# Performance work log

Hardware: AMD Instinct MI355X
Metric: run time of the kernel (lower is better)

## Reference

```python
import jax, jax.numpy as jnp
import numpy as np

K_HOPS = 2
IMPROVED = False  # self-loop fill weight = 1.0


def setup_inputs() -> dict:
    key = jax.random.key(0)
    k1, k2, k3 = jax.random.split(key, 3)
    n_nodes, n_edges, d_feat, units = 100000, 1600000, 64, 64
    x = jax.random.normal(k1, (n_nodes, d_feat), dtype=jnp.float32)
    edge_index = jax.random.randint(k2, (2, n_edges), 0, n_nodes, dtype=jnp.int32)
    edge_weight = jnp.ones((n_edges,), dtype=jnp.float32)
    kernel = jax.random.normal(k3, (d_feat, units), dtype=jnp.float32) * (1.0 / np.sqrt(d_feat))
    bias = jnp.zeros((units,), dtype=jnp.float32)
    return {"x": x, "edge_index": edge_index, "edge_weight": edge_weight,
            "kernel": kernel, "bias": bias}


def reference(x, edge_index, edge_weight, kernel, bias):
    n = x.shape[0]
    # renorm trick: add self-loops (fill=1, or 2 if improved) BEFORE normalization
    fill = jnp.float32(2.0 if IMPROVED else 1.0)
    loop_idx = jnp.arange(n, dtype=edge_index.dtype)
    row = jnp.concatenate([edge_index[0], loop_idx])
    col = jnp.concatenate([edge_index[1], loop_idx])
    w = jnp.concatenate([edge_weight, jnp.full((n,), fill, dtype=edge_weight.dtype)])
    # symmetric GCN normalization: D^{-1/2} A D^{-1/2}
    deg = jax.ops.segment_sum(w, row, num_segments=n)
    dinv = jnp.where(deg > 0, jax.lax.rsqrt(deg), 0.0)
    norm_w = dinv[row] * w * dinv[col]  # [n_edges + n]
    # K-hop propagation: gather source feats, scale, scatter-add to targets
    h = x
    for _ in range(K_HOPS):
        msgs = h[col] * norm_w[:, None]           # [E+n, d] gather + scale
        h = jax.ops.segment_sum(msgs, row, num_segments=n)  # scatter-add
    # final dense projection
    return h @ kernel + bias
```

## Files before the change

### kernel.cpp

```cpp
#include <hip/hip_runtime.h>

#define D 64

static __host__ __device__ inline int alignup(int x) { return (x + 63) & ~63; }

__device__ inline float blo(unsigned int u) { return __uint_as_float(u << 16); }
__device__ inline float bhi(unsigned int u) { return __uint_as_float(u & 0xffff0000u); }
__device__ inline unsigned short f2b(float f) {
    unsigned int u = __float_as_uint(f);
    return (unsigned short)((u + 0x7FFFu + ((u >> 16) & 1u)) >> 16);
}
__device__ inline unsigned int packb(float lo, float hi) {
    return (unsigned int)f2b(lo) | ((unsigned int)f2b(hi) << 16);
}

typedef short bf16x8 __attribute__((ext_vector_type(8)));
typedef float f32x4 __attribute__((ext_vector_type(4)));

__global__ void prep(const float* __restrict__ x, unsigned short* __restrict__ xb,
                     const float* __restrict__ W, unsigned short* __restrict__ wbt,
                     const int* __restrict__ row, int* __restrict__ bhist,
                     long nElem, int nbC, int E, int chunk, int NB) {
    int blk = (int)blockIdx.x;
    if (blk < nbC) {
        long t = (long)blk * blockDim.x + threadIdx.x;
        long i = t * 4;
        if (i + 3 < nElem) {
            float4 v = *(const float4*)(x + i);
            ushort4 o;
            o.x = f2b(v.x); o.y = f2b(v.y); o.z = f2b(v.z); o.w = f2b(v.w);
            *(ushort4*)(xb + i) = o;
        } else {
            for (long k = i; k < nElem; ++k) xb[k] = f2b(x[k]);
        }
        return;
    }
    if (blk < nbC + 16) {
        int idx = (blk - nbC) * 256 + threadIdx.x;
        int c = idx >> 6, k = idx & 63;
        wbt[c * 64 + k] = f2b(W[k * 64 + c]);
        return;
    }
    __shared__ int h[512];
    int b = blk - nbC - 16;
    for (int k = threadIdx.x; k < NB; k += blockDim.x) h[k] = 0;
    __syncthreads();
    int s = b * chunk, e = min(s + chunk, E);
    for (int p = s + (int)threadIdx.x; p < e; p += blockDim.x)
        atomicAdd(&h[row[p] >> 8], 1);
    __syncthreads();
    for (int k = threadIdx.x; k < NB; k += blockDim.x)
        bhist[k * 256 + b] = h[k];
}

__global__ void scanA(int* __restrict__ bhist, int* __restrict__ bcnt, int NB) {
    __shared__ int s[256];
    int k = blockIdx.x;
    int t = threadIdx.x;
    int v = bhist[k * 256 + t];
    s[t] = v;
    __syncthreads();
    for (int o = 1; o < 256; o <<= 1) {
        int u = (t >= o) ? s[t - o] : 0;
        __syncthreads();
        if (t >= o) s[t] += u;
        __syncthreads();
    }
    bhist[k * 256 + t] = s[t] - v;
    if (t == 255) bcnt[k] = s[t];
}

__global__ void scan_boff(const int* __restrict__ bcnt, int* __restrict__ boff, int nb) {
    __shared__ int s[512];
    int t = threadIdx.x;
    s[t] = (t < nb) ? bcnt[t] : 0;
    __syncthreads();
    for (int o = 1; o < 512; o <<= 1) {
        int v = (t >= o) ? s[t - o] : 0;
        __syncthreads();
        if (t >= o) s[t] += v;
        __syncthreads();
    }
    if (t < nb) boff[t] = (t == 0) ? 0 : s[t - 1];
}

__global__ void scatterB(const int* __restrict__ row, const int* __restrict__ col,
                         const float* __restrict__ w, const int* __restrict__ bhist,
                         const int* __restrict__ boff, uint2* __restrict__ ebuf,
                         int E, int chunk, int NB) {
    __shared__ int cur[512];
    int b = blockIdx.x;
    for (int k = threadIdx.x; k < NB; k += blockDim.x)
        cur[k] = boff[k] + bhist[k * 256 + b];
    __syncthreads();
    int s = b * chunk, e = min(s + chunk, E);
    for (int p = s + (int)threadIdx.x; p < e; p += blockDim.x) {
        int r = row[p];
        int bkt = r >> 8;
        int pos = atomicAdd(&cur[bkt], 1);
        ebuf[pos] = make_uint2(((unsigned)(r & 255) << 24) | (unsigned)col[p],
                               __float_as_uint(w[p]));
    }
}

__global__ void bucketC(const uint2* __restrict__ ebuf, const int* __restrict__ boff,
                        const int* __restrict__ bcnt, float* __restrict__ dinv,
                        int* __restrict__ off, int* __restrict__ endp,
                        uint2* __restrict__ csr, int n, float fill) {
    __shared__ int cntS[256];
    __shared__ float wsum[256];
    __shared__ int scanS[256];
    __shared__ int cur[256];
    int k = blockIdx.x;
    int t = threadIdx.x;
    cntS[t] = 0;
    wsum[t] = 0.f;
    __syncthreads();
    int s = boff[k], e = s + bcnt[k];
    for (int p = s + t; p < e; p += 256) {
        uint2 ent = ebuf[p];
        int rl = (int)(ent.x >> 24);
        atomicAdd(&cntS[rl], 1);
        atomicAdd(&wsum[rl], __uint_as_float(ent.y));
    }
    __syncthreads();
    int r = k * 256 + t;
    int v = cntS[t];
    if (r < n) {
        float d = fill + wsum[t];
        dinv[r] = d > 0.0f ? rsqrtf(d) : 0.0f;
    }
    scanS[t] = v;
    __syncthreads();
    for (int o = 1; o < 256; o <<= 1) {
        int u = (t >= o) ? scanS[t - o] : 0;
        __syncthreads();
        if (t >= o) scanS[t] += u;
        __syncthreads();
    }
    int base = boff[k] + scanS[t] - v;
    cur[t] = base;
    if (r < n) { off[r] = base; endp[r] = base + v; }
    __syncthreads();
    for (int p = s + t; p < e; p += 256) {
        uint2 ent = ebuf[p];
        int rl = (int)(ent.x >> 24);
        int pos = atomicAdd(&cur[rl], 1);
        csr[pos] = ent;
    }
}

__global__ void normB(uint2* __restrict__ csr, const int* __restrict__ boff,
                      const int* __restrict__ bcnt, const float* __restrict__ dinv, int n) {
    __shared__ float dl[256];
    int k = blockIdx.x;
    int t = threadIdx.x;
    int r = k * 256 + t;
    dl[t] = (r < n) ? dinv[r] : 0.f;
    __syncthreads();
    int s = boff[k], e = s + bcnt[k];
    for (int p = s + t; p < e; p += 256) {
        uint2 ent = csr[p];
        int rl = (int)(ent.x >> 24);
        unsigned c = ent.x & 0xFFFFFFu;
        float wn = __uint_as_float(ent.y) * dl[rl] * dinv[c];
        csr[p] = make_uint2(c, __float_as_uint(wn));
    }
}

__global__ void __launch_bounds__(256)
hop_g8(const unsigned short* __restrict__ xb, const float* __restrict__ dinv,
       const int* __restrict__ off, const int* __restrict__ end,
       const uint2* __restrict__ csr,
       unsigned short* __restrict__ outb, int n) {
    int t = blockIdx.x * blockDim.x + threadIdx.x;
    int wave = t >> 6;
    int lane = t & 63;
    int g = lane >> 3, q = lane & 7;
    int i = wave * 8 + g;
    bool active = i < n;
    int ii = active ? i : n - 1;

    const unsigned int* xw = (const unsigned int*)xb;
    float di = dinv[ii];
    float di2 = di * di;
    uint4 sv = *(const uint4*)(xw + (long)ii * 32 + q * 4);
    float a0 = blo(sv.x) * di2, a1 = bhi(sv.x) * di2;
    float a2 = blo(sv.y) * di2, a3 = bhi(sv.y) * di2;
    float a4 = blo(sv.z) * di2, a5 = bhi(sv.z) * di2;
    float a6 = blo(sv.w) * di2, a7 = bhi(sv.w) * di2;

    int s = active ? off[ii] : 0;
    int e = active ? end[ii] : 0;

    for (int b = s; b < e; b += 16) {
        int i0 = b + q;     if (i0 >= e) i0 = e - 1;
        int i1 = b + 8 + q; if (i1 >= e) i1 = e - 1;
        uint2 e0 = csr[i0];
        uint2 e1 = csr[i1];
        uint4 v[16];
        float wv[16];
        #pragma unroll
        for (int j = 0; j < 16; ++j) {
            int srcl = g * 8 + (j & 7);
            int cb = __shfl((int)(j < 8 ? e0.x : e1.x), srcl, 64);
            float wj = __uint_as_float(__shfl((int)(j < 8 ? e0.y : e1.y), srcl, 64));
            if (b + j >= e) wj = 0.0f;
            wv[j] = wj;
            v[j] = make_uint4(0u, 0u, 0u, 0u);
            if (wj != 0.0f) v[j] = *(const uint4*)(xw + (long)cb * 32 + q * 4);
        }
        #pragma unroll
        for (int j = 0; j < 16; ++j) {
            float wj = wv[j];
            a0 += blo(v[j].x) * wj; a1 += bhi(v[j].x) * wj;
            a2 += blo(v[j].y) * wj; a3 += bhi(v[j].y) * wj;
            a4 += blo(v[j].z) * wj; a5 += bhi(v[j].z) * wj;
            a6 += blo(v[j].w) * wj; a7 += bhi(v[j].w) * wj;
        }
    }

    if (!active) return;
    uint4 o;
    o.x = packb(a0, a1); o.y = packb(a2, a3);
    o.z = packb(a4, a5); o.w = packb(a6, a7);
    *(uint4*)((unsigned int*)outb + (long)i * 32 + q * 4) = o;
}

__global__ void __launch_bounds__(256)
proj_mfma(const unsigned short* __restrict__ h2b, const unsigned short* __restrict__ wbt,
          const float* __restrict__ bias, float* __restrict__ out, int n) {
    int lane = threadIdx.x & 63;
    int w = (blockIdx.x * blockDim.x + threadIdx.x) >> 6;
    int nTiles = (n + 15) >> 4;
    if (w >= nTiles) return;
    int r0 = w * 16;
    int rl = lane & 15;
    int half = lane >> 4;

    int ar = r0 + rl; if (ar >= n) ar = n - 1;
    const unsigned short* arow = h2b + (long)ar * 64 + half * 8;
    bf16x8 A0 = __builtin_bit_cast(bf16x8, *(const uint4*)(arow));
    bf16x8 A1 = __builtin_bit_cast(bf16x8, *(const uint4*)(arow + 32));

    #pragma unroll
    for (int t = 0; t < 4; ++t) {
        const unsigned short* bcol = wbt + (long)(t * 16 + rl) * 64 + half * 8;
        bf16x8 B0 = __builtin_bit_cast(bf16x8, *(const uint4*)(bcol));
        bf16x8 B1 = __builtin_bit_cast(bf16x8, *(const uint4*)(bcol + 32));
        float bl = bias[t * 16 + rl];
        f32x4 acc = {bl, bl, bl, bl};
        acc = __builtin_amdgcn_mfma_f32_16x16x32_bf16(A0, B0, acc, 0, 0, 0);
        acc = __builtin_amdgcn_mfma_f32_16x16x32_bf16(A1, B1, acc, 0, 0, 0);
        #pragma unroll
        for (int j = 0; j < 4; ++j) {
            int r = r0 + half * 4 + j;
            if (r < n) out[(long)r * 64 + t * 16 + rl] = acc[j];
        }
    }
}

extern "C" void kernel_launch(void* const* d_in, const int* in_sizes, int n_in,
                              void* d_out, int out_size, void* d_ws, size_t ws_size,
                              hipStream_t stream) {
    const float* x    = (const float*)d_in[0];
    const int*   ei   = (const int*)d_in[1];
    const float* ew   = (const float*)d_in[2];
    const float* W    = (const float*)d_in[3];
    const float* bias = (const float*)d_in[4];

    int n = in_sizes[0] / D;
    int E = in_sizes[2];
    const int* row = ei;
    const int* col = ei + E;

    float* out = (float*)d_out;

    const int NB = (n + 255) >> 8;
    const int BA = 256;
    int chunk = (E + BA - 1) / BA;

    float* dinv  = (float*)d_ws;
    int*   off   = (int*)(dinv + alignup(n));
    int*   endp  = off + alignup(n);
    int*   bcnt  = endp + alignup(n);
    int*   boff  = bcnt + 512;
    int*   bhist = boff + 512;
    uint2* csr   = (uint2*)(bhist + alignup(NB * 256));
    unsigned short* xb  = (unsigned short*)(csr + alignup(E));
    unsigned short* h1b = xb + (long)alignup(n) * D;
    unsigned short* h2b = h1b + (long)alignup(n) * D;
    unsigned short* wbt = h2b + (long)alignup(n) * D;
    uint2* ebuf = (uint2*)h2b;

    const float fill = 1.0f;
    const int blk = 256;

    long nElem = (long)n * D;
    int nbC = (int)((nElem / 4 + blk - 1) / blk);
    prep<<<nbC + 16 + BA, blk, 0, stream>>>(x, xb, W, wbt, row, bhist,
                                            nElem, nbC, E, chunk, NB);

    scanA<<<NB, 256, 0, stream>>>(bhist, bcnt, NB);
    scan_boff<<<1, 512, 0, stream>>>(bcnt, boff, NB);
    scatterB<<<BA, 256, 0, stream>>>(row, col, ew, bhist, boff, ebuf, E, chunk, NB);
    bucketC<<<NB, 256, 0, stream>>>(ebuf, boff, bcnt, dinv, off, endp, csr, n, fill);
    normB<<<NB, 256, 0, stream>>>(csr, boff, bcnt, dinv, n);

    int nWaves = (n + 7) / 8;
    int nbHop = (nWaves * 64 + blk - 1) / blk;
    hop_g8<<<nbHop, blk, 0, stream>>>(xb, dinv, off, endp, csr, h1b, n);
    hop_g8<<<nbHop, blk, 0, stream>>>(h1b, dinv, off, endp, csr, h2b, n);

    int nTiles = (n + 15) / 16;
    int nbProj = (nTiles * 64 + blk - 1) / blk;
    proj_mfma<<<nbProj, blk, 0, stream>>>(h2b, wbt, bias, out, n);
}
```

Measured before the change: 160.0 us.

## Fuse bucket scans via last-block pattern and merge CSR placement with normalization

Merges the per-bucket scan and the global bucket-offset scan into one kernel, where the last block to finish (tracked by an atomic counter reset in prep) computes the offsets. Splits bucketC so it only computes degrees and row offsets; a new placeN kernel then places each edge into CSR order and writes its normalized weight in the same pass. This removes one kernel launch and the separate read-modify-write pass over the CSR array, at the cost of a 512-thread scan kernel with a threadfence and atomic handoff.

```diff
diff --git a/kernel.cpp b/kernel.cpp
--- a/kernel.cpp
+++ b/kernel.cpp
@@ -20,6 +20,7 @@
 __global__ void prep(const float* __restrict__ x, unsigned short* __restrict__ xb,
                      const float* __restrict__ W, unsigned short* __restrict__ wbt,
                      const int* __restrict__ row, int* __restrict__ bhist,
+                     int* __restrict__ done,
                      long nElem, int nbC, int E, int chunk, int NB) {
     int blk = (int)blockIdx.x;
     if (blk < nbC) {
@@ -36,6 +37,7 @@
         return;
     }
     if (blk < nbC + 16) {
+        if (blk == nbC && threadIdx.x == 0) *done = 0;
         int idx = (blk - nbC) * 256 + threadIdx.x;
         int c = idx >> 6, k = idx & 63;
         wbt[c * 64 + k] = f2b(W[k * 64 + c]);
@@ -53,35 +55,43 @@
         bhist[k * 256 + b] = h[k];
 }
 
-__global__ void scanA(int* __restrict__ bhist, int* __restrict__ bcnt, int NB) {
+__global__ void scanAB(int* __restrict__ bhist, int* __restrict__ bcnt,
+                       int* __restrict__ boff, int NB, int* __restrict__ done) {
     __shared__ int s[256];
+    __shared__ int sb[512];
+    __shared__ int isLast;
     int k = blockIdx.x;
     int t = threadIdx.x;
-    int v = bhist[k * 256 + t];
-    s[t] = v;
+    int v = 0;
+    if (t < 256) {
+        v = bhist[k * 256 + t];
+        s[t] = v;
+    }
     __syncthreads();
     for (int o = 1; o < 256; o <<= 1) {
-        int u = (t >= o) ? s[t - o] : 0;
-        __syncthreads();
-        if (t >= o) s[t] += u;
-        __syncthreads();
-    }
-    bhist[k * 256 + t] = s[t] - v;
-    if (t == 255) bcnt[k] = s[t];
-}
-
-__global__ void scan_boff(const int* __restrict__ bcnt, int* __restrict__ boff, int nb) {
-    __shared__ int s[512];
-    int t = threadIdx.x;
-    s[t] = (t < nb) ? bcnt[t] : 0;
+        int u = 0;
+        if (t < 256 && t >= o) u = s[t - o];
+        __syncthreads();
+        if (t < 256 && t >= o) s[t] += u;
+        __syncthreads();
+    }
+    if (t < 256) bhist[k * 256 + t] = s[t] - v;
+    if (t == 255) atomicExch(&bcnt[k], s[255]);
+    __threadfence();
+    __syncthreads();
+    if (t == 0) isLast = (atomicAdd(done, 1) == NB - 1);
+    __syncthreads();
+    if (!isLast) return;
+    int v2 = (t < NB) ? atomicAdd(&bcnt[t], 0) : 0;
+    sb[t] = v2;
     __syncthreads();
     for (int o = 1; o < 512; o <<= 1) {
-        int v = (t >= o) ? s[t - o] : 0;
-        __syncthreads();
-        if (t >= o) s[t] += v;
-        __syncthreads();
-    }
-    if (t < nb) boff[t] = (t == 0) ? 0 : s[t - 1];
+        int u = (t >= o) ? sb[t - o] : 0;
+        __syncthreads();
+        if (t >= o) sb[t] += u;
+        __syncthreads();
+    }
+    if (t < NB) boff[t] = sb[t] - v2;
 }
 
 __global__ void scatterB(const int* __restrict__ row, const int* __restrict__ col,
@@ -106,11 +116,10 @@
 __global__ void bucketC(const uint2* __restrict__ ebuf, const int* __restrict__ boff,
                         const int* __restrict__ bcnt, float* __restrict__ dinv,
                         int* __restrict__ off, int* __restrict__ endp,
-                        uint2* __restrict__ csr, int n, float fill) {
+                        int n, float fill) {
     __shared__ int cntS[256];
     __shared__ float wsum[256];
     __shared__ int scanS[256];
-    __shared__ int cur[256];
     int k = blockIdx.x;
     int t = threadIdx.x;
     cntS[t] = 0;
@@ -126,45 +135,42 @@
     __syncthreads();
     int r = k * 256 + t;
     int v = cntS[t];
+    scanS[t] = v;
+    __syncthreads();
+    for (int o = 1; o < 256; o <<= 1) {
+        int u = (t >= o) ? scanS[t - o] : 0;
+        __syncthreads();
+        if (t >= o) scanS[t] += u;
+        __syncthreads();
+    }
     if (r < n) {
         float d = fill + wsum[t];
         dinv[r] = d > 0.0f ? rsqrtf(d) : 0.0f;
-    }
-    scanS[t] = v;
-    __syncthreads();
-    for (int o = 1; o < 256; o <<= 1) {
-        int u = (t >= o) ? scanS[t - o] : 0;
-        __syncthreads();
-        if (t >= o) scanS[t] += u;
-        __syncthreads();
-    }
-    int base = boff[k] + scanS[t] - v;
-    cur[t] = base;
-    if (r < n) { off[r] = base; endp[r] = base + v; }
-    __syncthreads();
-    for (int p = s + t; p < e; p += 256) {
-        uint2 ent = ebuf[p];
-        int rl = (int)(ent.x >> 24);
-        int pos = atomicAdd(&cur[rl], 1);
-        csr[pos] = ent;
-    }
-}
-
-__global__ void normB(uint2* __restrict__ csr, const int* __restrict__ boff,
-                      const int* __restrict__ bcnt, const float* __restrict__ dinv, int n) {
+        int base = boff[k] + scanS[t] - v;
+        off[r] = base;
+        endp[r] = base + v;
+    }
+}
+
+__global__ void placeN(const uint2* __restrict__ ebuf, const int* __restrict__ boff,
+                       const int* __restrict__ bcnt, const float* __restrict__ dinv,
+                       const int* __restrict__ off, uint2* __restrict__ csr, int n) {
     __shared__ float dl[256];
+    __shared__ int cur[256];
     int k = blockIdx.x;
     int t = threadIdx.x;
     int r = k * 256 + t;
     dl[t] = (r < n) ? dinv[r] : 0.f;
+    cur[t] = (r < n) ? off[r] : 0;
     __syncthreads();
     int s = boff[k], e = s + bcnt[k];
     for (int p = s + t; p < e; p += 256) {
-        uint2 ent = csr[p];
+        uint2 ent = ebuf[p];
         int rl = (int)(ent.x >> 24);
         unsigned c = ent.x & 0xFFFFFFu;
+        int pos = atomicAdd(&cur[rl], 1);
         float wn = __uint_as_float(ent.y) * dl[rl] * dinv[c];
-        csr[p] = make_uint2(c, __float_as_uint(wn));
+        csr[pos] = make_uint2(c, __float_as_uint(wn));
     }
 }
 
@@ -285,7 +291,8 @@
     int*   endp  = off + alignup(n);
     int*   bcnt  = endp + alignup(n);
     int*   boff  = bcnt + 512;
-    int*   bhist = boff + 512;
+    int*   done  = boff + 512;
+    int*   bhist = done + 64;
     uint2* csr   = (uint2*)(bhist + alignup(NB * 256));
     unsigned short* xb  = (unsigned short*)(csr + alignup(E));
     unsigned short* h1b = xb + (long)alignup(n) * D;
@@ -298,14 +305,13 @@
 
     long nElem = (long)n * D;
     int nbC = (int)((nElem / 4 + blk - 1) / blk);
-    prep<<<nbC + 16 + BA, blk, 0, stream>>>(x, xb, W, wbt, row, bhist,
+    prep<<<nbC + 16 + BA, blk, 0, stream>>>(x, xb, W, wbt, row, bhist, done,
                                             nElem, nbC, E, chunk, NB);
 
-    scanA<<<NB, 256, 0, stream>>>(bhist, bcnt, NB);
-    scan_boff<<<1, 512, 0, stream>>>(bcnt, boff, NB);
+    scanAB<<<NB, 512, 0, stream>>>(bhist, bcnt, boff, NB, done);
     scatterB<<<BA, 256, 0, stream>>>(row, col, ew, bhist, boff, ebuf, E, chunk, NB);
-    bucketC<<<NB, 256, 0, stream>>>(ebuf, boff, bcnt, dinv, off, endp, csr, n, fill);
-    normB<<<NB, 256, 0, stream>>>(csr, boff, bcnt, dinv, n);
+    bucketC<<<NB, 256, 0, stream>>>(ebuf, boff, bcnt, dinv, off, endp, n, fill);
+    placeN<<<NB, 256, 0, stream>>>(ebuf, boff, bcnt, dinv, off, csr, n);
 
     int nWaves = (n + 7) / 8;
     int nbHop = (nWaves * 64 + blk - 1) / blk;
```

After: 201.9 us. 26.1% more time.
